# Kernel optimization log

Measured on AMD Instinct MI355X. Metric: run time of the kernel, lower is better.

Reference implementation:

```python
import jax, jax.numpy as jnp
from jax import lax
import numpy as np

EPS = 1e-12  # matches torch F.normalize eps


def _dtw_similarity(s1, s2):
    # s1: [L1, D], s2: [L2, D]
    L1, L2 = s1.shape[0], s2.shape[0]
    s1n = s1 / jnp.maximum(jnp.linalg.norm(s1, axis=1, keepdims=True), EPS)
    s2n = s2 / jnp.maximum(jnp.linalg.norm(s2, axis=1, keepdims=True), EPS)
    dist = 1.0 - s1n @ s2n.T  # [L1, L2] cosine distance

    # DTW DP. Row 0 is a cumsum; each subsequent row has a left-to-right
    # sequential dependency handled by an inner scan.
    row0 = jnp.cumsum(dist[0])

    def row_step(prev_row, d_row):
        # prev_row: dtw[i-1, :], d_row: dist[i, :]
        first = prev_row[0] + d_row[0]  # dtw[i, 0]
        # min(prev[j], prev[j-1]) for j >= 1 (vectorized part of the min)
        p = jnp.minimum(prev_row[1:], prev_row[:-1])

        def col_step(c, inp):
            dj, pj = inp
            new = dj + jnp.minimum(pj, c)  # c = dtw[i, j-1]
            return new, new

        _, rest = lax.scan(col_step, first, (d_row[1:], p))
        new_row = jnp.concatenate([first[None], rest])
        return new_row, None

    last_row, _ = lax.scan(row_step, row0, dist[1:])
    dtw_distance = last_row[-1]
    normalized = dtw_distance / (L1 + L2)
    return 1.0 / (1.0 + normalized)


def setup_inputs() -> dict:
    key = jax.random.key(0)
    k1, k2 = jax.random.split(key)
    seq1 = jax.random.normal(k1, (16, 1024, 768), dtype=jnp.float32)
    seq2 = jax.random.normal(k2, (16, 1024, 768), dtype=jnp.float32)
    return {"seq1": seq1, "seq2": seq2}


def reference(seq1, seq2):
    # seq1: [B, L1, D], seq2: [B, L2, D] -> [B]
    return jax.vmap(_dtw_similarity)(seq1, seq2)
```

## Files before the change

### kernel.cpp

```cpp
#include <hip/hip_runtime.h>
#include <hip/hip_bf16.h>

typedef __attribute__((ext_vector_type(4))) float f32x4;
typedef __attribute__((ext_vector_type(8))) short bf16x8;

#define DINF 1e30f

__device__ __forceinline__ unsigned short f2bf(float f) {
    unsigned int u = __builtin_bit_cast(unsigned int, f);
    u += 0x7FFFu + ((u >> 16) & 1u);
    return (unsigned short)(u >> 16);
}

__global__ __launch_bounds__(256) void norm_bf16_kernel(
    const float* __restrict__ s1, const float* __restrict__ s2,
    __hip_bfloat16* __restrict__ o1, __hip_bfloat16* __restrict__ o2) {
    const int gb = blockIdx.x;
    const float* in;
    __hip_bfloat16* out;
    int rowbase;
    if (gb < 4096) { in = s1; out = o1; rowbase = gb * 4; }
    else           { in = s2; out = o2; rowbase = (gb - 4096) * 4; }
    const int wv = threadIdx.x >> 6;
    const int l  = threadIdx.x & 63;
    const int row = rowbase + wv;

    const float* rp = in + (size_t)row * 768 + l * 4;
    float4 x0 = *(const float4*)(rp);
    float4 x1 = *(const float4*)(rp + 256);
    float4 x2 = *(const float4*)(rp + 512);

    float s = x0.x*x0.x + x0.y*x0.y + x0.z*x0.z + x0.w*x0.w
            + x1.x*x1.x + x1.y*x1.y + x1.z*x1.z + x1.w*x1.w
            + x2.x*x2.x + x2.y*x2.y + x2.z*x2.z + x2.w*x2.w;
#pragma unroll
    for (int off = 32; off > 0; off >>= 1) s += __shfl_xor(s, off, 64);

    const float inv = 1.0f / fmaxf(sqrtf(s), 1e-12f);

    __hip_bfloat16* op = out + (size_t)row * 768 + l * 4;
    ushort4 o;
    o.x = f2bf(x0.x*inv); o.y = f2bf(x0.y*inv); o.z = f2bf(x0.z*inv); o.w = f2bf(x0.w*inv);
    *(ushort4*)(op) = o;
    o.x = f2bf(x1.x*inv); o.y = f2bf(x1.y*inv); o.z = f2bf(x1.z*inv); o.w = f2bf(x1.w*inv);
    *(ushort4*)(op + 256) = o;
    o.x = f2bf(x2.x*inv); o.y = f2bf(x2.y*inv); o.z = f2bf(x2.z*inv); o.w = f2bf(x2.w*inv);
    *(ushort4*)(op + 512) = o;
}

#define GLOAD_LDS16(g, l)                                                      \
    __builtin_amdgcn_global_load_lds(                                          \
        (const __attribute__((address_space(1))) void*)(g),                    \
        (__attribute__((address_space(3))) void*)(l), 16, 0, 0)

__global__ __launch_bounds__(256) void gemm_dist_kernel(
    const __hip_bfloat16* __restrict__ A, const __hip_bfloat16* __restrict__ B,
    float* __restrict__ dist) {
    __shared__ __hip_bfloat16 lA[128 * 64];
    __shared__ __hip_bfloat16 lB[128 * 64];

    const int blk  = (blockIdx.x & 7) * 128 + (blockIdx.x >> 3);
    const int b    = blk >> 6;
    const int tile = blk & 63;
    const int tm = tile >> 3, tn = tile & 7;
    const int tid  = threadIdx.x;
    const int lane = tid & 63, w = tid >> 6;
    const int lr = lane & 15, lg = lane >> 4;
    const int wm = w >> 1, wn = w & 1;

    const __hip_bfloat16* Ab = A + (size_t)b * (1024 * 768) + (size_t)(tm * 128) * 768;
    const __hip_bfloat16* Bb = B + (size_t)b * (1024 * 768) + (size_t)(tn * 128) * 768;

    const int srow = tid >> 3;
    const int scol = (tid & 7) * 8;

    char* lAb = (char*)lA;
    char* lBb = (char*)lB;

    f32x4 acc[4][4];
#pragma unroll
    for (int m = 0; m < 4; ++m)
#pragma unroll
        for (int n = 0; n < 4; ++n) acc[m][n] = (f32x4){0.f, 0.f, 0.f, 0.f};

    for (int k0 = 0; k0 < 768; k0 += 64) {
#pragma unroll
        for (int q = 0; q < 4; ++q) {
            GLOAD_LDS16(Ab + (size_t)(q * 32 + srow) * 768 + k0 + scol,
                        lAb + q * 4096 + w * 1024);
            GLOAD_LDS16(Bb + (size_t)(q * 32 + srow) * 768 + k0 + scol,
                        lBb + q * 4096 + w * 1024);
        }
        __syncthreads();

#pragma unroll
        for (int ks = 0; ks < 64; ks += 32) {
            bf16x8 af[4], bfr[4];
#pragma unroll
            for (int m = 0; m < 4; ++m)
                af[m] = *(const bf16x8*)&lA[(wm * 64 + m * 16 + lr) * 64 + ks + lg * 8];
#pragma unroll
            for (int n = 0; n < 4; ++n)
                bfr[n] = *(const bf16x8*)&lB[(wn * 64 + n * 16 + lr) * 64 + ks + lg * 8];
#pragma unroll
            for (int m = 0; m < 4; ++m)
#pragma unroll
                for (int n = 0; n < 4; ++n)
                    acc[m][n] = __builtin_amdgcn_mfma_f32_16x16x32_bf16(af[m], bfr[n], acc[m][n], 0, 0, 0);
        }
        __syncthreads();
    }

    float* Drow = dist + (size_t)b * (1024 * 1024);
#pragma unroll
    for (int m = 0; m < 4; ++m)
#pragma unroll
        for (int n = 0; n < 4; ++n)
#pragma unroll
            for (int r = 0; r < 4; ++r) {
                const int row = tm * 128 + wm * 64 + m * 16 + lg * 4 + r;
                const int col = tn * 128 + wn * 64 + n * 16 + lr;
                Drow[(size_t)row * 1024 + col] = 1.0f - acc[m][n][r];
            }
}


#define DECLB(N) float4 N##_0, N##_1, N##_2, N##_3

#define LOADB(N, kk) do {                                                      \
    int r_ = (kk) - 2 * t;                                                     \
    r_ = r_ < 0 ? 0 : (r_ > 1023 ? 1023 : r_);                                 \
    const float4* p_ = (const float4*)(Db + ((size_t)r_ << 10));               \
    N##_0 = p_[0]; N##_1 = p_[1]; N##_2 = p_[2]; N##_3 = p_[3];                \
} while (0)

#define STEPBODY(N, E0EXPR) do {                                               \
    float e0_ = (E0EXPR);                                                      \
    float c0_  = N##_0.x + e0_;                                                \
    float c1_  = N##_0.y + fminf(fminf(p1,  p0),  c0_);                        \
    float c2_  = N##_0.z + fminf(fminf(p2,  p1),  c1_);                        \
    float c3_  = N##_0.w + fminf(fminf(p3,  p2),  c2_);                        \
    float c4_  = N##_1.x + fminf(fminf(p4,  p3),  c3_);                        \
    float c5_  = N##_1.y + fminf(fminf(p5,  p4),  c4_);                        \
    float c6_  = N##_1.z + fminf(fminf(p6,  p5),  c5_);                        \
    float c7_  = N##_1.w + fminf(fminf(p7,  p6),  c6_);                        \
    float c8_  = N##_2.x + fminf(fminf(p8,  p7),  c7_);                        \
    float c9_  = N##_2.y + fminf(fminf(p9,  p8),  c8_);                        \
    float c10_ = N##_2.z + fminf(fminf(p10, p9),  c9_);                        \
    float c11_ = N##_2.w + fminf(fminf(p11, p10), c10_);                       \
    float c12_ = N##_3.x + fminf(fminf(p12, p11), c11_);                       \
    float c13_ = N##_3.y + fminf(fminf(p13, p12), c12_);                       \
    float c14_ = N##_3.z + fminf(fminf(p14, p13), c13_);                       \
    float c15_ = N##_3.w + fminf(fminf(p15, p14), c14_);                       \
    p0=c0_; p1=c1_; p2=c2_; p3=c3_; p4=c4_; p5=c5_; p6=c6_; p7=c7_;            \
    p8=c8_; p9=c9_; p10=c10_; p11=c11_; p12=c12_; p13=c13_; p14=c14_; p15=c15_;\
    a3 = a2; a2 = a1;                                                          \
    a1 = __shfl_up(c15_, 1, 64);                                               \
    a1 = lane0 ? DINF : a1;                                                    \
} while (0)

#define STEPB(N)       STEPBODY(N, fminf(fminf(p0, a3), a2))
#define STEPB_FIRST(N) STEPBODY(N, lane0 ? 0.0f : fminf(fminf(p0, a3), a2))

__global__ __launch_bounds__(64) void dtw_dp_kernel(
    const float* __restrict__ dist, float* __restrict__ out) {
    const int b = blockIdx.x;
    const int t = threadIdx.x;
    const bool lane0 = (t == 0);
    const float* Db = dist + ((size_t)b << 20) + t * 16;

    float p0 = DINF, p1 = DINF, p2 = DINF, p3 = DINF,
          p4 = DINF, p5 = DINF, p6 = DINF, p7 = DINF,
          p8 = DINF, p9 = DINF, p10 = DINF, p11 = DINF,
          p12 = DINF, p13 = DINF, p14 = DINF, p15 = DINF;
    float a1 = DINF, a2 = DINF, a3 = DINF;

    DECLB(A); DECLB(B); DECLB(C); DECLB(D);
    DECLB(E); DECLB(F); DECLB(G); DECLB(H);

    LOADB(A, 0); LOADB(B, 1); LOADB(C, 2); LOADB(D, 3);
    LOADB(E, 4); LOADB(F, 5); LOADB(G, 6); LOADB(H, 7);

    STEPB_FIRST(A); LOADB(A, 8);
    STEPB(B); LOADB(B, 9);
    STEPB(C); LOADB(C, 10);
    STEPB(D); LOADB(D, 11);
    STEPB(E); LOADB(E, 12);
    STEPB(F); LOADB(F, 13);
    STEPB(G); LOADB(G, 14);
    STEPB(H); LOADB(H, 15);

#pragma unroll 1
    for (int k = 8; k < 1144; k += 8) {
        STEPB(A); LOADB(A, k + 8);
        STEPB(B); LOADB(B, k + 9);
        STEPB(C); LOADB(C, k + 10);
        STEPB(D); LOADB(D, k + 11);
        STEPB(E); LOADB(E, k + 12);
        STEPB(F); LOADB(F, k + 13);
        STEPB(G); LOADB(G, k + 14);
        STEPB(H); LOADB(H, k + 15);
    }

    STEPB(A); STEPB(B); STEPB(C); STEPB(D); STEPB(E); STEPB(F);

    if (t == 63) out[b] = 1.0f / (1.0f + p15 * (1.0f / 2048.0f));
}

extern "C" void kernel_launch(void* const* d_in, const int* in_sizes, int n_in,
                              void* d_out, int out_size, void* d_ws, size_t ws_size,
                              hipStream_t stream) {
    const float* s1 = (const float*)d_in[0];
    const float* s2 = (const float*)d_in[1];
    float* out = (float*)d_out;

    char* ws = (char*)d_ws;
    __hip_bfloat16* Abf = (__hip_bfloat16*)(ws);
    __hip_bfloat16* Bbf = (__hip_bfloat16*)(ws + 25165824);
    float* dist = (float*)(ws + 50331648);

    norm_bf16_kernel<<<8192, 256, 0, stream>>>(s1, s2, Abf, Bbf);
    gemm_dist_kernel<<<16 * 64, 256, 0, stream>>>(Abf, Bbf, dist);
    dtw_dp_kernel<<<16, 64, 0, stream>>>(dist, out);
}
```

Baseline: 258.6 us.

## Stream DTW wavefront tiles via global-to-LDS DMA ring buffer

The DP wavefront kernel now prefetches its per-lane dist tiles with global_load_lds into an 8-slot shared-memory ring, then reads each slot into registers one step ahead. This replaces the eight register-resident float4 buffers, with explicit vmcnt/lgkmcnt waits to keep loads in flight. The aim is to cut register pressure and keep memory latency off the serial dependency chain. It adds LDS traffic and hand-tuned wait counts, which could be fragile or add stalls.

After: 528.1 us. +104.2%, slower.

```diff
diff --git a/kernel.cpp b/kernel.cpp
--- a/kernel.cpp
+++ b/kernel.cpp
@@ -125,33 +125,47 @@
 }
 
 
-#define DECLB(N) float4 N##_0, N##_1, N##_2, N##_3
-
-#define LOADB(N, kk) do {                                                      \
-    int r_ = (kk) - 2 * t;                                                     \
+#define LGKM0    asm volatile("s_waitcnt lgkmcnt(0)" ::: "memory")
+#define VWAIT(n) asm volatile("s_waitcnt vmcnt(" #n ")" ::: "memory")
+
+#define GLDMA16(g, l)                                                          \
+    __builtin_amdgcn_global_load_lds(                                          \
+        (const __attribute__((address_space(1))) void*)(g),                    \
+        (__attribute__((address_space(3))) void*)(l), 16, 0, 0)
+
+#define LOADB(kk, SLOT) do {                                                   \
+    int r_ = (kk) - tt;                                                        \
     r_ = r_ < 0 ? 0 : (r_ > 1023 ? 1023 : r_);                                 \
-    const float4* p_ = (const float4*)(Db + ((size_t)r_ << 10));               \
-    N##_0 = p_[0]; N##_1 = p_[1]; N##_2 = p_[2]; N##_3 = p_[3];                \
+    const char* g_ = DbB + ((size_t)r_ << 12);                                 \
+    GLDMA16(g_,      &ring[SLOT][0][0]);                                       \
+    GLDMA16(g_ + 16, &ring[SLOT][1][0]);                                       \
+    GLDMA16(g_ + 32, &ring[SLOT][2][0]);                                       \
+    GLDMA16(g_ + 48, &ring[SLOT][3][0]);                                       \
 } while (0)
 
-#define STEPBODY(N, E0EXPR) do {                                               \
+#define DSREAD(S, P) do {                                                      \
+    P##_0 = ring[S][0][t]; P##_1 = ring[S][1][t];                              \
+    P##_2 = ring[S][2][t]; P##_3 = ring[S][3][t];                              \
+} while (0)
+
+#define STEPBODY(P, E0EXPR) do {                                               \
     float e0_ = (E0EXPR);                                                      \
-    float c0_  = N##_0.x + e0_;                                                \
-    float c1_  = N##_0.y + fminf(fminf(p1,  p0),  c0_);                        \
-    float c2_  = N##_0.z + fminf(fminf(p2,  p1),  c1_);                        \
-    float c3_  = N##_0.w + fminf(fminf(p3,  p2),  c2_);                        \
-    float c4_  = N##_1.x + fminf(fminf(p4,  p3),  c3_);                        \
-    float c5_  = N##_1.y + fminf(fminf(p5,  p4),  c4_);                        \
-    float c6_  = N##_1.z + fminf(fminf(p6,  p5),  c5_);                        \
-    float c7_  = N##_1.w + fminf(fminf(p7,  p6),  c6_);                        \
-    float c8_  = N##_2.x + fminf(fminf(p8,  p7),  c7_);                        \
-    float c9_  = N##_2.y + fminf(fminf(p9,  p8),  c8_);                        \
-    float c10_ = N##_2.z + fminf(fminf(p10, p9),  c9_);                        \
-    float c11_ = N##_2.w + fminf(fminf(p11, p10), c10_);                       \
-    float c12_ = N##_3.x + fminf(fminf(p12, p11), c11_);                       \
-    float c13_ = N##_3.y + fminf(fminf(p13, p12), c12_);                       \
-    float c14_ = N##_3.z + fminf(fminf(p14, p13), c13_);                       \
-    float c15_ = N##_3.w + fminf(fminf(p15, p14), c14_);                       \
+    float c0_  = P##_0.x + e0_;                                                \
+    float c1_  = P##_0.y + fminf(fminf(p1,  p0),  c0_);                        \
+    float c2_  = P##_0.z + fminf(fminf(p2,  p1),  c1_);                        \
+    float c3_  = P##_0.w + fminf(fminf(p3,  p2),  c2_);                        \
+    float c4_  = P##_1.x + fminf(fminf(p4,  p3),  c3_);                        \
+    float c5_  = P##_1.y + fminf(fminf(p5,  p4),  c4_);                        \
+    float c6_  = P##_1.z + fminf(fminf(p6,  p5),  c5_);                        \
+    float c7_  = P##_1.w + fminf(fminf(p7,  p6),  c6_);                        \
+    float c8_  = P##_2.x + fminf(fminf(p8,  p7),  c7_);                        \
+    float c9_  = P##_2.y + fminf(fminf(p9,  p8),  c8_);                        \
+    float c10_ = P##_2.z + fminf(fminf(p10, p9),  c9_);                        \
+    float c11_ = P##_2.w + fminf(fminf(p11, p10), c10_);                       \
+    float c12_ = P##_3.x + fminf(fminf(p12, p11), c11_);                       \
+    float c13_ = P##_3.y + fminf(fminf(p13, p12), c12_);                       \
+    float c14_ = P##_3.z + fminf(fminf(p14, p13), c13_);                       \
+    float c15_ = P##_3.w + fminf(fminf(p15, p14), c14_);                       \
     p0=c0_; p1=c1_; p2=c2_; p3=c3_; p4=c4_; p5=c5_; p6=c6_; p7=c7_;            \
     p8=c8_; p9=c9_; p10=c10_; p11=c11_; p12=c12_; p13=c13_; p14=c14_; p15=c15_;\
     a3 = a2; a2 = a1;                                                          \
@@ -159,15 +173,18 @@
     a1 = lane0 ? DINF : a1;                                                    \
 } while (0)
 
-#define STEPB(N)       STEPBODY(N, fminf(fminf(p0, a3), a2))
-#define STEPB_FIRST(N) STEPBODY(N, lane0 ? 0.0f : fminf(fminf(p0, a3), a2))
+#define STEPB(P)       STEPBODY(P, fminf(fminf(p0, a3), a2))
+#define STEPB_FIRST(P) STEPBODY(P, lane0 ? 0.0f : fminf(fminf(p0, a3), a2))
 
 __global__ __launch_bounds__(64) void dtw_dp_kernel(
     const float* __restrict__ dist, float* __restrict__ out) {
+    __shared__ float4 ring[8][4][64];
+
     const int b = blockIdx.x;
     const int t = threadIdx.x;
+    const int tt = 2 * t;
     const bool lane0 = (t == 0);
-    const float* Db = dist + ((size_t)b << 20) + t * 16;
+    const char* DbB = (const char*)(dist + ((size_t)b << 20)) + t * 64;
 
     float p0 = DINF, p1 = DINF, p2 = DINF, p3 = DINF,
           p4 = DINF, p5 = DINF, p6 = DINF, p7 = DINF,
@@ -175,34 +192,50 @@
           p12 = DINF, p13 = DINF, p14 = DINF, p15 = DINF;
     float a1 = DINF, a2 = DINF, a3 = DINF;
 
-    DECLB(A); DECLB(B); DECLB(C); DECLB(D);
-    DECLB(E); DECLB(F); DECLB(G); DECLB(H);
-
-    LOADB(A, 0); LOADB(B, 1); LOADB(C, 2); LOADB(D, 3);
-    LOADB(E, 4); LOADB(F, 5); LOADB(G, 6); LOADB(H, 7);
-
-    STEPB_FIRST(A); LOADB(A, 8);
-    STEPB(B); LOADB(B, 9);
-    STEPB(C); LOADB(C, 10);
-    STEPB(D); LOADB(D, 11);
-    STEPB(E); LOADB(E, 12);
-    STEPB(F); LOADB(F, 13);
-    STEPB(G); LOADB(G, 14);
-    STEPB(H); LOADB(H, 15);
+    float4 X_0, X_1, X_2, X_3;
+    float4 Y_0, Y_1, Y_2, Y_3;
+
+    LOADB(0, 0); LOADB(1, 1); LOADB(2, 2); LOADB(3, 3);
+    LOADB(4, 4); LOADB(5, 5); LOADB(6, 6); LOADB(7, 7);
+    VWAIT(28);
+    DSREAD(0, X);
+
+    LGKM0; LOADB(8,  0); VWAIT(28); DSREAD(1, Y); STEPB_FIRST(X);
+    LGKM0; LOADB(9,  1); VWAIT(28); DSREAD(2, X); STEPB(Y);
+    LGKM0; LOADB(10, 2); VWAIT(28); DSREAD(3, Y); STEPB(X);
+    LGKM0; LOADB(11, 3); VWAIT(28); DSREAD(4, X); STEPB(Y);
+    LGKM0; LOADB(12, 4); VWAIT(28); DSREAD(5, Y); STEPB(X);
+    LGKM0; LOADB(13, 5); VWAIT(28); DSREAD(6, X); STEPB(Y);
+    LGKM0; LOADB(14, 6); VWAIT(28); DSREAD(7, Y); STEPB(X);
+    LGKM0; LOADB(15, 7); VWAIT(28); DSREAD(0, X); STEPB(Y);
 
 #pragma unroll 1
-    for (int k = 8; k < 1144; k += 8) {
-        STEPB(A); LOADB(A, k + 8);
-        STEPB(B); LOADB(B, k + 9);
-        STEPB(C); LOADB(C, k + 10);
-        STEPB(D); LOADB(D, k + 11);
-        STEPB(E); LOADB(E, k + 12);
-        STEPB(F); LOADB(F, k + 13);
-        STEPB(G); LOADB(G, k + 14);
-        STEPB(H); LOADB(H, k + 15);
+    for (int k = 8; k < 1136; k += 8) {
+        LGKM0; LOADB(k + 8,  0); VWAIT(28); DSREAD(1, Y); STEPB(X);
+        LGKM0; LOADB(k + 9,  1); VWAIT(28); DSREAD(2, X); STEPB(Y);
+        LGKM0; LOADB(k + 10, 2); VWAIT(28); DSREAD(3, Y); STEPB(X);
+        LGKM0; LOADB(k + 11, 3); VWAIT(28); DSREAD(4, X); STEPB(Y);
+        LGKM0; LOADB(k + 12, 4); VWAIT(28); DSREAD(5, Y); STEPB(X);
+        LGKM0; LOADB(k + 13, 5); VWAIT(28); DSREAD(6, X); STEPB(Y);
+        LGKM0; LOADB(k + 14, 6); VWAIT(28); DSREAD(7, Y); STEPB(X);
+        LGKM0; LOADB(k + 15, 7); VWAIT(28); DSREAD(0, X); STEPB(Y);
     }
 
-    STEPB(A); STEPB(B); STEPB(C); STEPB(D); STEPB(E); STEPB(F);
+    LGKM0; LOADB(1144, 0); VWAIT(28); DSREAD(1, Y); STEPB(X);
+    LGKM0; LOADB(1145, 1); VWAIT(28); DSREAD(2, X); STEPB(Y);
+    LGKM0; LOADB(1146, 2); VWAIT(28); DSREAD(3, Y); STEPB(X);
+    LGKM0; LOADB(1147, 3); VWAIT(28); DSREAD(4, X); STEPB(Y);
+    LGKM0; LOADB(1148, 4); VWAIT(28); DSREAD(5, Y); STEPB(X);
+    LGKM0; LOADB(1149, 5); VWAIT(28); DSREAD(6, X); STEPB(Y);
+
+    VWAIT(24); DSREAD(7, Y); STEPB(X);
+    VWAIT(20); DSREAD(0, X); STEPB(Y);
+    VWAIT(16); DSREAD(1, Y); STEPB(X);
+    VWAIT(12); DSREAD(2, X); STEPB(Y);
+    VWAIT(8);  DSREAD(3, Y); STEPB(X);
+    VWAIT(4);  DSREAD(4, X); STEPB(Y);
+    VWAIT(0);  DSREAD(5, Y); STEPB(X);
+    STEPB(Y);
 
     if (t == 63) out[b] = 1.0f / (1.0f + p15 * (1.0f / 2048.0f));
 }
```
